# Optimization experiments

Measured on AMD Instinct MI355X. Metric: run time of the kernel, lower is better.

The kernel has to match this reference:

```python
import jax, jax.numpy as jnp
import numpy as np

B, Nq, C, H = 1, 300, 256, 8
h, w = 32, 32
HW = h * w
HID = 512  # rpe_hidden_dim
HD = C // H


def setup_inputs() -> dict:
    key = jax.random.key(0)
    ks = jax.random.split(key, 16)
    s = 0.02
    inp = {
        "raw_query": jax.random.normal(ks[0], (B, Nq, C), jnp.float32),
        "query_pos": jax.random.normal(ks[1], (B, Nq, C), jnp.float32),
        "reference_points": jax.random.uniform(ks[2], (B, Nq, 2), jnp.float32),
        "raw_src": jax.random.normal(ks[3], (B, HW, C), jnp.float32),
        "src_pos_embed": jax.random.normal(ks[4], (B, HW, C), jnp.float32),
        "Wq": jax.random.normal(ks[5], (C, C), jnp.float32) * s,
        "bq": jnp.zeros((C,), jnp.float32),
        "Wk": jax.random.normal(ks[6], (C, C), jnp.float32) * s,
        "bk": jnp.zeros((C,), jnp.float32),
        "Wv": jax.random.normal(ks[7], (C, C), jnp.float32) * s,
        "bv": jnp.zeros((C,), jnp.float32),
        "Wo": jax.random.normal(ks[8], (C, C), jnp.float32) * s,
        "bo": jnp.zeros((C,), jnp.float32),
        "W1": jax.random.normal(ks[9], (HID, 2), jnp.float32),   # cpb MLP layer 1
        "b1": jnp.zeros((HID,), jnp.float32),
        "W2": jax.random.normal(ks[10], (H, HID), jnp.float32) * s,  # cpb MLP layer 2 (no bias)
        "input_spatial_shapes": np.array([[h, w]], dtype=np.int64),
    }
    return inp


def _key_positions(hh, ww):
    ys = (jnp.arange(hh, dtype=jnp.float32) + 0.5) / hh
    xs = (jnp.arange(ww, dtype=jnp.float32) + 0.5) / ww
    yy, xx = jnp.meshgrid(ys, xs, indexing="ij")  # row-major: idx = y*w + x
    return jnp.stack([xx.ravel(), yy.ravel()], axis=-1)  # [HW, 2] (x, y)


def reference(raw_query, query_pos, reference_points, raw_src, src_pos_embed,
              Wq, bq, Wk, bk, Wv, bv, Wo, bo, W1, b1, W2, input_spatial_shapes):
    hh, ww = int(input_spatial_shapes[0, 0]), int(input_spatial_shapes[0, 1])
    scale = HD ** (-0.5)
    queries = raw_query + query_pos                      # [B,Nq,C]
    memory = raw_src + src_pos_embed                     # [B,HW,C]

    q = (queries @ Wq.T + bq).reshape(B, Nq, H, HD)
    k = (memory @ Wk.T + bk).reshape(B, hh * ww, H, HD)
    v = (memory @ Wv.T + bv).reshape(B, hh * ww, H, HD)

    logits = jnp.einsum("bqhd,bkhd->bhqk", q, k) * scale  # [B,H,Nq,HW]

    key_pos = _key_positions(hh, ww)                      # [HW,2]
    delta = reference_points[:, :, None, :] - key_pos[None, None]  # [B,Nq,HW,2]
    hid = jax.nn.relu(jnp.einsum("bqkc,hc->bqkh", delta, W1) + b1)  # [B,Nq,HW,HID]
    bias = jnp.einsum("bqkf,hf->bhqk", hid, W2)           # [B,H,Nq,HW]

    attn = jax.nn.softmax(logits + bias, axis=-1)
    out = jnp.einsum("bhqk,bkhd->bqhd", attn, v).reshape(B, Nq, C)
    return out @ Wo.T + bo
```

## Files before the change

kernel.cpp:

```cpp
#include <hip/hip_runtime.h>
#include <hip/hip_fp16.h>
#include <stdint.h>

#define NQ   300
#define CDIM 256
#define NH   8
#define HD   32
#define HWK  1024
#define HIDD 512

typedef __attribute__((ext_vector_type(8))) _Float16 f16x8;
typedef __attribute__((ext_vector_type(2))) _Float16 h2v;
typedef __attribute__((ext_vector_type(4))) float f32x4;

#define QB_OFF   0
#define KB_OFF   153600
#define VT_OFF   677888
#define PO_OFF   1202176
#define PL_OFF   3659776

__device__ __forceinline__ short f16b(float x){
  _Float16 h = (_Float16)x;
  return __builtin_bit_cast(short, h);
}

__device__ __forceinline__ h2v cvt2h(float a, float b){
  auto r = __builtin_amdgcn_cvt_pkrtz(a, b);
  return __builtin_bit_cast(h2v, r);
}

__device__ __forceinline__ uint32_t pk_f16(float a, float b){
  auto r = __builtin_amdgcn_cvt_pkrtz(a, b);
  return __builtin_bit_cast(uint32_t, r);
}

__global__ __launch_bounds__(256) void proj_kernel(
    const float* __restrict__ rq, const float* __restrict__ qp,
    const float* __restrict__ rs, const float* __restrict__ spe,
    const float* __restrict__ Wq, const float* __restrict__ bq,
    const float* __restrict__ Wk, const float* __restrict__ bk,
    const float* __restrict__ Wv, const float* __restrict__ bv,
    const float* __restrict__ Wo, const float* __restrict__ bo,
    char* __restrict__ ws, float* __restrict__ dout, int final_mode)
{
  int bxid = blockIdx.x;
  int tile = bxid >> 1, half = bxid & 1;
  const float *in1, *in2, *W, *bias;
  int r0, M, mode;
  const float* po = (const float*)(ws + PO_OFF);
  const float* pl = (const float*)(ws + PL_OFF);
  if (final_mode){
    in1 = po; in2 = nullptr; W = Wo; bias = bo;
    r0 = tile*16; M = NQ; mode = 3;
  } else if (tile < 19){
    in1 = rq; in2 = qp; W = Wq; bias = bq; r0 = tile*16; M = NQ; mode = 0;
  } else if (tile < 83){
    in1 = rs; in2 = spe; W = Wk; bias = bk; r0 = (tile-19)*16; M = HWK; mode = 1;
  } else {
    in1 = rs; in2 = spe; W = Wv; bias = bv; r0 = (tile-83)*16; M = HWK; mode = 2;
  }
  __shared__ __align__(16) float At[32][20];
  __shared__ float Wl[32][129];
  __shared__ float linv[16][8];
  int tid = threadIdx.x;
  int n_loc = tid & 127;
  int rg = tid >> 7;
  int n = half*128 + n_loc;
  float acc[8];
  float bv_ = bias[n];
  #pragma unroll
  for (int i=0;i<8;i++) acc[i] = bv_;

  if (mode == 3 && tid < 128){
    int r = tid >> 3, hh = tid & 7;
    int gr = r0 + r; if (gr >= M) gr = M - 1;
    float s = 0.f;
    #pragma unroll
    for (int p = 0; p < 8; p++) s += pl[((size_t)p*NQ+gr)*NH+hh];
    linv[r][hh] = 1.0f / s;
  }

  for (int c0 = 0; c0 < CDIM; c0 += 32){
    __syncthreads();
    for (int e = tid; e < 512; e += 256){
      int r = e >> 5, c = e & 31;
      int gr = r0 + r; if (gr >= M) gr = M - 1;
      float v;
      if (mode == 3){
        int cc = c0 + c;
        v = 0.f;
        #pragma unroll
        for (int p = 0; p < 8; p++) v += po[(size_t)(p*NQ+gr)*CDIM + cc];
        v *= linv[r][c0 >> 5];
      } else {
        v = in1[gr*CDIM + c0 + c];
        if (in2) v += in2[gr*CDIM + c0 + c];
      }
      At[c][r] = v;
    }
    for (int e = tid; e < 4096; e += 256){
      int c = e & 31, nn = e >> 5;
      Wl[c][nn] = W[(half*128 + nn)*CDIM + c0 + c];
    }
    __syncthreads();
    #pragma unroll
    for (int c = 0; c < 32; c++){
      float w = Wl[c][n_loc];
      const float4* ap = (const float4*)&At[c][rg*8];
      float4 a0 = ap[0], a1 = ap[1];
      acc[0] = fmaf(a0.x, w, acc[0]);
      acc[1] = fmaf(a0.y, w, acc[1]);
      acc[2] = fmaf(a0.z, w, acc[2]);
      acc[3] = fmaf(a0.w, w, acc[3]);
      acc[4] = fmaf(a1.x, w, acc[4]);
      acc[5] = fmaf(a1.y, w, acc[5]);
      acc[6] = fmaf(a1.z, w, acc[6]);
      acc[7] = fmaf(a1.w, w, acc[7]);
    }
  }

  if (mode == 0){
    short* qb = (short*)(ws + QB_OFF);
    const float s = 0.17677669529663687f;
    #pragma unroll
    for (int i=0;i<8;i++){
      int gr = r0 + rg*8 + i;
      if (gr < M) qb[gr*CDIM + n] = f16b(acc[i]*s);
    }
  } else if (mode == 1){
    short* kb = (short*)(ws + KB_OFF);
    int h = n >> 5, d = n & 31;
    #pragma unroll
    for (int i=0;i<8;i++){
      int gr = r0 + rg*8 + i;
      if (gr < M) kb[((size_t)h*HWK + gr)*HD + d] = f16b(acc[i]);
    }
  } else if (mode == 2){
    short* vt = (short*)(ws + VT_OFF);
    uint32_t p[4];
    #pragma unroll
    for (int i=0;i<4;i++) p[i] = pk_f16(acc[2*i], acc[2*i+1]);
    *(uint4*)(vt + n*HWK + r0 + rg*8) = make_uint4(p[0], p[1], p[2], p[3]);
  } else {
    #pragma unroll
    for (int i=0;i<8;i++){
      int gr = r0 + rg*8 + i;
      if (gr < M) dout[gr*CDIM + n] = acc[i];
    }
  }
}

__global__ __launch_bounds__(256, 4) void fused_kernel(
    const float* __restrict__ refp, const float* __restrict__ W1,
    const float* __restrict__ b1, const float* __restrict__ W2,
    const short* __restrict__ qb, const short* __restrict__ kb,
    const short* __restrict__ vt, float* __restrict__ po,
    float* __restrict__ pl)
{
  int bid = blockIdx.x;
  int q = bid >> 3, kr = bid & 7;
  int tid = threadIdx.x, wave = tid >> 6, lane = tid & 63;
  int n = lane & 15, qd = lane >> 4;

  __shared__ __align__(16) _Float16 nwx[HIDD];
  __shared__ __align__(16) _Float16 c1s[4][HIDD];
  __shared__ __align__(16) _Float16 w2l[NH][520];
  __shared__ __align__(16) _Float16 pb[NH][136];
  __shared__ __align__(16) float part[4][NH][32];
  __shared__ float lsum[4][NH];

  float rx = refp[2*q], ry = refp[2*q+1];
  {
    int f0 = tid * 2;
    float4 w = *(const float4*)(W1 + 2*f0);
    float2 bb = *(const float2*)(b1 + f0);
    float a0 = fmaf(w.x, rx, fmaf(w.y, ry, bb.x));
    float a1 = fmaf(w.z, rx, fmaf(w.w, ry, bb.y));
    *(h2v*)&nwx[f0] = cvt2h(-w.x, -w.z);
    #pragma unroll
    for (int r = 0; r < 4; r++){
      float ky = ((float)(kr*4 + r) + 0.5f) * (1.0f/32.0f);
      float c0 = fmaf(-w.y, ky, a0);
      float c1 = fmaf(-w.w, ky, a1);
      *(h2v*)&c1s[r][f0] = cvt2h(c0, c1);
    }
  }
  for (int e = tid; e < 2048; e += 256){
    int r = e >> 8, j = e & 255;
    float2 x = *(const float2*)(W2 + r*HIDD + 2*j);
    *(h2v*)&w2l[r][2*j] = cvt2h(x.x, x.y);
  }
  f16x8 qfrag;
  if (n < NH) qfrag = *(const f16x8*)(qb + q*CDIM + n*HD + qd*8);
  else { f16x8 z = {0,0,0,0,0,0,0,0}; qfrag = z; }
  f16x8 qm[NH];
  #pragma unroll
  for (int h = 0; h < NH; h++){
    f16x8 z = {0,0,0,0,0,0,0,0};
    qm[h] = (n == h) ? qfrag : z;
  }
  __syncthreads();

  const int kyrow = kr*4 + wave;
  const int kbase = kyrow * 32;

  f32x4 acc[2];
  #pragma unroll
  for (int t = 0; t < 2; t++){
    int k0 = kbase + t*16;
    f32x4 d = {0.f,0.f,0.f,0.f};
    #pragma unroll
    for (int h = 0; h < NH; h++){
      f16x8 af = *(const f16x8*)(kb + ((size_t)h*HWK + k0 + n)*HD + qd*8);
      d = __builtin_amdgcn_mfma_f32_16x16x32_f16(af, qm[h], d, 0, 0, 0);
    }
    acc[t] = d;
  }

  _Float16 kxAh = (_Float16)(((float)n + 0.5f) * (1.0f/32.0f));
  _Float16 kxBh = (_Float16)(((float)n + 16.5f) * (1.0f/32.0f));
  f16x8 kxA8, kxB8, z8;
  #pragma unroll
  for (int j = 0; j < 8; j++){ kxA8[j] = kxAh; kxB8[j] = kxBh; z8[j] = (_Float16)0.f; }
  const _Float16* c1r = &c1s[wave][0];
  #pragma unroll 4
  for (int kc = 0; kc < 16; kc++){
    int f0 = kc*32 + qd*8;
    f16x8 c1v = *(const f16x8*)(c1r + f0);
    f16x8 wxv = *(const f16x8*)(&nwx[f0]);
    f16x8 bfr = *(const f16x8*)(&w2l[n & 7][f0]);
    #pragma unroll
    for (int t = 0; t < 2; t++){
      f16x8 kx8 = t ? kxB8 : kxA8;
      f16x8 e = __builtin_elementwise_max(wxv * kx8 + c1v, z8);
      acc[t] = __builtin_amdgcn_mfma_f32_16x16x32_f16(e, bfr, acc[t], 0, 0, 0);
    }
  }

  float lacc = 0.f;
  #pragma unroll
  for (int t = 0; t < 2; t++){
    float e0 = __expf(acc[t][0]);
    float e1 = __expf(acc[t][1]);
    float e2 = __expf(acc[t][2]);
    float e3 = __expf(acc[t][3]);
    if (n < NH){
      uint2 p2;
      p2.x = pk_f16(e0, e1);
      p2.y = pk_f16(e2, e3);
      *(uint2*)&pb[n][wave*32 + t*16 + qd*4] = p2;
    }
    float s = e0 + e1 + e2 + e3;
    s += __shfl_xor(s, 16);
    s += __shfl_xor(s, 32);
    lacc += s;
  }
  if (lane < NH) lsum[wave][lane] = lacc;

  #pragma unroll
  for (int h = 0; h < NH; h++){
    int kl = wave*32 + qd*8;
    f16x8 pa = *(const f16x8*)&pb[h][kl];
    f16x8 v0 = *(const f16x8*)(vt + ((size_t)(h*HD +      n))*HWK + kr*128 + kl);
    f16x8 v1 = *(const f16x8*)(vt + ((size_t)(h*HD + 16 + n))*HWK + kr*128 + kl);
    f32x4 o0 = {0.f,0.f,0.f,0.f}, o1 = {0.f,0.f,0.f,0.f};
    o0 = __builtin_amdgcn_mfma_f32_16x16x32_f16(pa, v0, o0, 0, 0, 0);
    o1 = __builtin_amdgcn_mfma_f32_16x16x32_f16(pa, v1, o1, 0, 0, 0);
    if (qd == 0){
      part[wave][h][n]      = o0[0];
      part[wave][h][16 + n] = o1[0];
    }
  }
  __syncthreads();

  {
    int h = tid >> 5, d = tid & 31;
    float s = part[0][h][d] + part[1][h][d] + part[2][h][d] + part[3][h][d];
    po[((size_t)kr*NQ + q)*CDIM + tid] = s;
    if (tid < NH)
      pl[((size_t)kr*NQ + q)*NH + tid] =
          lsum[0][tid] + lsum[1][tid] + lsum[2][tid] + lsum[3][tid];
  }
}

extern "C" void kernel_launch(void* const* d_in, const int* in_sizes, int n_in,
                              void* d_out, int out_size, void* d_ws, size_t ws_size,
                              hipStream_t stream)
{
  const float* rq  = (const float*)d_in[0];
  const float* qp  = (const float*)d_in[1];
  const float* rp  = (const float*)d_in[2];
  const float* rs  = (const float*)d_in[3];
  const float* spe = (const float*)d_in[4];
  const float* Wq  = (const float*)d_in[5];
  const float* bq  = (const float*)d_in[6];
  const float* Wk  = (const float*)d_in[7];
  const float* bk  = (const float*)d_in[8];
  const float* Wv  = (const float*)d_in[9];
  const float* bv  = (const float*)d_in[10];
  const float* Wo  = (const float*)d_in[11];
  const float* bo  = (const float*)d_in[12];
  const float* W1  = (const float*)d_in[13];
  const float* b1  = (const float*)d_in[14];
  const float* W2  = (const float*)d_in[15];
  char* ws = (char*)d_ws;
  float* dout = (float*)d_out;

  proj_kernel<<<294, 256, 0, stream>>>(rq, qp, rs, spe, Wq, bq, Wk, bk,
      Wv, bv, Wo, bo, ws, dout, 0);
  fused_kernel<<<2400, 256, 0, stream>>>(rp, W1, b1, W2,
      (const short*)(ws + QB_OFF), (const short*)(ws + KB_OFF),
      (const short*)(ws + VT_OFF), (float*)(ws + PO_OFF),
      (float*)(ws + PL_OFF));
  proj_kernel<<<38, 256, 0, stream>>>(rq, qp, rs, spe, Wq, bq, Wk, bk,
      Wv, bv, Wo, bo, ws, dout, 1);
}
```

Before: 165.7 us.

## Drop in-block partial reduction; write per-wave partials and add combine kernel

The fused attention kernel no longer reduces the four waves' partial outputs and row sums through shared memory with a barrier. Each wave now writes its own partial directly to a 32-slice workspace, and the occupancy hint rises from 4 to 6 blocks per CU. A new combine kernel sums the 32 slices, normalises by the summed softmax denominators, and hands a ready buffer to the output projection. The cost is four times more partial-output traffic to global memory and an extra kernel launch.

```diff
diff --git a/kernel.cpp b/kernel.cpp
--- a/kernel.cpp
+++ b/kernel.cpp
@@ -17,7 +17,8 @@
 #define KB_OFF   153600
 #define VT_OFF   677888
 #define PO_OFF   1202176
-#define PL_OFF   3659776
+#define PL_OFF   11032576
+#define OB_OFF   11339776
 
 __device__ __forceinline__ short f16b(float x){
   _Float16 h = (_Float16)x;
@@ -47,10 +48,8 @@
   int tile = bxid >> 1, half = bxid & 1;
   const float *in1, *in2, *W, *bias;
   int r0, M, mode;
-  const float* po = (const float*)(ws + PO_OFF);
-  const float* pl = (const float*)(ws + PL_OFF);
   if (final_mode){
-    in1 = po; in2 = nullptr; W = Wo; bias = bo;
+    in1 = (const float*)(ws + OB_OFF); in2 = nullptr; W = Wo; bias = bo;
     r0 = tile*16; M = NQ; mode = 3;
   } else if (tile < 19){
     in1 = rq; in2 = qp; W = Wq; bias = bq; r0 = tile*16; M = NQ; mode = 0;
@@ -61,7 +60,6 @@
   }
   __shared__ __align__(16) float At[32][20];
   __shared__ float Wl[32][129];
-  __shared__ float linv[16][8];
   int tid = threadIdx.x;
   int n_loc = tid & 127;
   int rg = tid >> 7;
@@ -71,31 +69,13 @@
   #pragma unroll
   for (int i=0;i<8;i++) acc[i] = bv_;
 
-  if (mode == 3 && tid < 128){
-    int r = tid >> 3, hh = tid & 7;
-    int gr = r0 + r; if (gr >= M) gr = M - 1;
-    float s = 0.f;
-    #pragma unroll
-    for (int p = 0; p < 8; p++) s += pl[((size_t)p*NQ+gr)*NH+hh];
-    linv[r][hh] = 1.0f / s;
-  }
-
   for (int c0 = 0; c0 < CDIM; c0 += 32){
     __syncthreads();
     for (int e = tid; e < 512; e += 256){
       int r = e >> 5, c = e & 31;
       int gr = r0 + r; if (gr >= M) gr = M - 1;
-      float v;
-      if (mode == 3){
-        int cc = c0 + c;
-        v = 0.f;
-        #pragma unroll
-        for (int p = 0; p < 8; p++) v += po[(size_t)(p*NQ+gr)*CDIM + cc];
-        v *= linv[r][c0 >> 5];
-      } else {
-        v = in1[gr*CDIM + c0 + c];
-        if (in2) v += in2[gr*CDIM + c0 + c];
-      }
+      float v = in1[gr*CDIM + c0 + c];
+      if (in2) v += in2[gr*CDIM + c0 + c];
       At[c][r] = v;
     }
     for (int e = tid; e < 4096; e += 256){
@@ -150,7 +130,7 @@
   }
 }
 
-__global__ __launch_bounds__(256, 4) void fused_kernel(
+__global__ __launch_bounds__(256, 6) void fused_kernel(
     const float* __restrict__ refp, const float* __restrict__ W1,
     const float* __restrict__ b1, const float* __restrict__ W2,
     const short* __restrict__ qb, const short* __restrict__ kb,
@@ -166,8 +146,6 @@
   __shared__ __align__(16) _Float16 c1s[4][HIDD];
   __shared__ __align__(16) _Float16 w2l[NH][520];
   __shared__ __align__(16) _Float16 pb[NH][136];
-  __shared__ __align__(16) float part[4][NH][32];
-  __shared__ float lsum[4][NH];
 
   float rx = refp[2*q], ry = refp[2*q+1];
   {
@@ -203,6 +181,7 @@
 
   const int kyrow = kr*4 + wave;
   const int kbase = kyrow * 32;
+  const int sl = kyrow;
 
   f32x4 acc[2];
   #pragma unroll
@@ -255,8 +234,9 @@
     s += __shfl_xor(s, 32);
     lacc += s;
   }
-  if (lane < NH) lsum[wave][lane] = lacc;
-
+  if (lane < NH) pl[((size_t)sl*NQ + q)*NH + lane] = lacc;
+
+  float* porow = po + ((size_t)sl*NQ + q)*CDIM;
   #pragma unroll
   for (int h = 0; h < NH; h++){
     int kl = wave*32 + qd*8;
@@ -267,20 +247,29 @@
     o0 = __builtin_amdgcn_mfma_f32_16x16x32_f16(pa, v0, o0, 0, 0, 0);
     o1 = __builtin_amdgcn_mfma_f32_16x16x32_f16(pa, v1, o1, 0, 0, 0);
     if (qd == 0){
-      part[wave][h][n]      = o0[0];
-      part[wave][h][16 + n] = o1[0];
-    }
+      porow[h*HD +      n] = o0[0];
+      porow[h*HD + 16 + n] = o1[0];
+    }
+  }
+}
+
+__global__ __launch_bounds__(256) void comb_kernel(
+    const float* __restrict__ po, const float* __restrict__ pl,
+    float* __restrict__ ob)
+{
+  int q = blockIdx.x, tid = threadIdx.x;
+  __shared__ float linv[NH];
+  if (tid < NH){
+    float s = 0.f;
+    #pragma unroll 8
+    for (int p = 0; p < 32; p++) s += pl[((size_t)p*NQ + q)*NH + tid];
+    linv[tid] = 1.0f / s;
   }
   __syncthreads();
-
-  {
-    int h = tid >> 5, d = tid & 31;
-    float s = part[0][h][d] + part[1][h][d] + part[2][h][d] + part[3][h][d];
-    po[((size_t)kr*NQ + q)*CDIM + tid] = s;
-    if (tid < NH)
-      pl[((size_t)kr*NQ + q)*NH + tid] =
-          lsum[0][tid] + lsum[1][tid] + lsum[2][tid] + lsum[3][tid];
-  }
+  float v = 0.f;
+  #pragma unroll 8
+  for (int p = 0; p < 32; p++) v += po[((size_t)p*NQ + q)*CDIM + tid];
+  ob[q*CDIM + tid] = v * linv[tid >> 5];
 }
 
 extern "C" void kernel_launch(void* const* d_in, const int* in_sizes, int n_in,
@@ -312,6 +301,8 @@
       (const short*)(ws + QB_OFF), (const short*)(ws + KB_OFF),
       (const short*)(ws + VT_OFF), (float*)(ws + PO_OFF),
       (float*)(ws + PL_OFF));
+  comb_kernel<<<300, 256, 0, stream>>>((const float*)(ws + PO_OFF),
+      (const float*)(ws + PL_OFF), (float*)(ws + OB_OFF));
   proj_kernel<<<38, 256, 0, stream>>>(rq, qp, rs, spe, Wq, bq, Wk, bk,
       Wv, bv, Wo, bo, ws, dout, 1);
 }
```

Result: slower. 170.4 us (+2.8%).
